# Kernel tuning notes

Measured on AMD Instinct MI355X. Metric: run time of the kernel, lower is better.

The kernel has to match this reference:

```python
import jax, jax.numpy as jnp
import numpy as np

B, N, M, K = 1, 200000, 100000, 16
C_IN, C_OUT, GFL, HEADS = 64, 128, 32, 8
C4 = C_OUT // 4          # 32, unary1 bottleneck width
C_MID = 16               # weightnet output channels


def _lin(key, fan_in, fan_out):
    return jax.random.normal(key, (fan_in, fan_out), jnp.float32) / np.sqrt(fan_in)


def setup_inputs() -> dict:
    key = jax.random.key(0)
    ks = jax.random.split(key, 20)
    return {
        'dense_xyz': jax.random.normal(ks[0], (B, N, 3), jnp.float32),
        'dense_feats': jax.random.normal(ks[1], (B, N, C_IN), jnp.float32),
        'dense_xyz_norm': jax.random.normal(ks[2], (B, N, 3), jnp.float32),
        'sparse_xyz': jax.random.normal(ks[3], (B, M, 3), jnp.float32),
        'sparse_xyz_norm': jax.random.normal(ks[4], (B, M, 3), jnp.float32),
        'vi_features': jax.random.normal(ks[5], (B, M, K, 12), jnp.float32),
        'nei_inds': jax.random.randint(ks[6], (B, M, K), 0, N),
        # unary1: in -> out/4 (Linear + BN(eval,init) + LeakyReLU(0.1))
        'w_unary1': _lin(ks[7], C_IN, C4), 'b_unary1': jnp.zeros((C4,), jnp.float32),
        # guidance_unary: out/4 -> GFL, no relu
        'w_gu': _lin(ks[8], C4, GFL), 'b_gu': jnp.zeros((GFL,), jnp.float32),
        # mlp_conv: 12 -> GFL (positional encoding on VI features)
        'w_pe': _lin(ks[9], 12, GFL), 'b_pe': jnp.zeros((GFL,), jnp.float32),
        # MultiHeadGuidance (subtraction): 2*GFL -> 8 -> HEADS
        'w_g1': _lin(ks[10], 2 * GFL, 8), 'b_g1': jnp.zeros((8,), jnp.float32),
        'w_g2': _lin(ks[11], 8, HEADS), 'b_g2': jnp.zeros((HEADS,), jnp.float32),
        # WeightNet: 12 -> 8 -> 8 -> 16, relu after each
        'w_wn1': _lin(ks[12], 12, 8), 'b_wn1': jnp.zeros((8,), jnp.float32),
        'w_wn2': _lin(ks[13], 8, 8), 'b_wn2': jnp.zeros((8,), jnp.float32),
        'w_wn3': _lin(ks[14], 8, C_MID), 'b_wn3': jnp.zeros((C_MID,), jnp.float32),
        # linear: out/4 * C_MID -> out/2
        'w_lin': _lin(ks[15], C4 * C_MID, C_OUT // 2), 'b_lin': jnp.zeros((C_OUT // 2,), jnp.float32),
        # unary2: out/2 -> out, no relu
        'w_u2': _lin(ks[16], C_OUT // 2, C_OUT), 'b_u2': jnp.zeros((C_OUT,), jnp.float32),
        # unary_shortcut: in -> out, no relu
        'w_sc': _lin(ks[17], C_IN, C_OUT), 'b_sc': jnp.zeros((C_OUT,), jnp.float32),
    }


def _gather(points, idx):
    # points: [B, N, C], idx: [B, M, K] int -> [B, M, K, C]
    return jax.vmap(lambda p, i: p[i])(points, idx)


def reference(dense_xyz, dense_feats, dense_xyz_norm, sparse_xyz, sparse_xyz_norm,
              vi_features, nei_inds,
              w_unary1, b_unary1, w_gu, b_gu, w_pe, b_pe,
              w_g1, b_g1, w_g2, b_g2,
              w_wn1, b_wn1, w_wn2, b_wn2, w_wn3, b_wn3,
              w_lin, b_lin, w_u2, b_u2, w_sc, b_sc):
    b, m, k = nei_inds.shape
    # unary1 (Linear+BN@init folds to Linear, LeakyReLU 0.1)
    feats_x = jax.nn.leaky_relu(dense_feats @ w_unary1 + b_unary1, 0.1)  # [B,N,C4]
    # USE_VI=True with precomputed vi_features -> weightNetInput = vi_features
    weightnet_input = vi_features                                        # [B,M,K,12]
    feat_pe = jax.nn.relu(weightnet_input @ w_pe + b_pe)                 # [B,M,K,GFL]
    guidance_x = feats_x @ w_gu + b_gu                                   # [B,N,GFL] (no_relu)
    gathered_g = _gather(guidance_x, nei_inds)                           # [B,M,K,GFL]
    g_feat = jnp.concatenate([gathered_g, feat_pe], axis=-1)             # [B,M,K,2*GFL]
    # subtraction guidance: query - max-pooled key over neighborhood
    scores = g_feat - jnp.max(g_feat, axis=2, keepdims=True)
    scores = jax.nn.relu(scores @ w_g1 + b_g1)
    scores = jax.nn.sigmoid(scores @ w_g2 + b_g2)                        # [B,M,K,H]
    gathered_feat = _gather(feats_x, nei_inds)                           # [B,M,K,C4]
    nf = gathered_feat.reshape(b, m, k, HEADS, C4 // HEADS) * scores[..., None]
    nf = nf.reshape(b, m, k, C4)
    # WeightNet on VI features
    w = jax.nn.relu(weightnet_input @ w_wn1 + b_wn1)
    w = jax.nn.relu(w @ w_wn2 + b_wn2)
    w = jax.nn.relu(w @ w_wn3 + b_wn3)                                   # [B,M,K,C_MID]
    # weighted neighbor aggregation: feat^T @ weights per point
    agg = jnp.einsum('bmkc,bmkw->bmcw', nf, w).reshape(b, m, C4 * C_MID)
    out = jax.nn.relu(agg @ w_lin + b_lin)                               # [B,M,out/2]
    out = out @ w_u2 + b_u2                                              # unary2, no relu
    # strided shortcut: max-pool dense feats over neighborhood, then unary
    sparse_feats = jnp.max(_gather(dense_feats, nei_inds), axis=2)       # [B,M,C_IN]
    shortcut = sparse_feats @ w_sc + b_sc
    return jax.nn.leaky_relu(out + shortcut, 0.1)                        # [B,M,C_OUT]
```

## Files before the change

### kernel.cpp

```cpp
#include <hip/hip_runtime.h>
#include <math.h>

typedef __attribute__((ext_vector_type(8))) __bf16 bf16x8;
typedef __attribute__((ext_vector_type(4))) __bf16 bf16x4;
typedef __attribute__((ext_vector_type(4))) float f32x4;
typedef __attribute__((ext_vector_type(8))) unsigned short ushort8;
typedef __attribute__((ext_vector_type(2))) _Float16 h2;

__device__ __forceinline__ float fdot2(h2 a, h2 b, float c) {
#if __has_builtin(__builtin_amdgcn_fdot2)
    return __builtin_amdgcn_fdot2(a, b, c, false);
#else
    return c + (float)a[0] * (float)b[0] + (float)a[1] * (float)b[1];
#endif
}

__device__ __forceinline__ h2 h2max(h2 a, h2 b) {
#if __has_builtin(__builtin_elementwise_max)
    return __builtin_elementwise_max(a, b);
#else
    h2 r; r[0] = a[0] > b[0] ? a[0] : b[0]; r[1] = a[1] > b[1] ? a[1] : b[1]; return r;
#endif
}

__device__ __forceinline__ h2 rowmax16h(h2 x) {
    int xi = __builtin_bit_cast(int, x);
    int y;
    y = __builtin_amdgcn_update_dpp(0, xi, 0x128, 0xf, 0xf, true);
    x = h2max(x, __builtin_bit_cast(h2, y)); xi = __builtin_bit_cast(int, x);
    y = __builtin_amdgcn_update_dpp(0, xi, 0x124, 0xf, 0xf, true);
    x = h2max(x, __builtin_bit_cast(h2, y)); xi = __builtin_bit_cast(int, x);
    y = __builtin_amdgcn_update_dpp(0, xi, 0x122, 0xf, 0xf, true);
    x = h2max(x, __builtin_bit_cast(h2, y)); xi = __builtin_bit_cast(int, x);
    y = __builtin_amdgcn_update_dpp(0, xi, 0x121, 0xf, 0xf, true);
    x = h2max(x, __builtin_bit_cast(h2, y));
    return x;
}

__device__ __forceinline__ unsigned int packh2(float a, float b) {
    h2 v = { (_Float16)a, (_Float16)b };
    return __builtin_bit_cast(unsigned int, v);
}

__global__ void prep_kernel(const float* __restrict__ wlin,
                            const float* __restrict__ wu2,
                            const float* __restrict__ wsc,
                            const float* __restrict__ w1,
                            const float* __restrict__ wg,
                            const float* __restrict__ wg1,
                            const float* __restrict__ wpe,
                            const float* __restrict__ wn1,
                            const float* __restrict__ wn2,
                            const float* __restrict__ wn3,
                            const float* __restrict__ wg2,
                            __bf16* __restrict__ wlinT,
                            __bf16* __restrict__ wu2T,
                            __bf16* __restrict__ wscT,
                            __bf16* __restrict__ w1Th,
                            __bf16* __restrict__ w1Tl,
                            __bf16* __restrict__ wgT,
                            unsigned int* __restrict__ pk)
{
    const int B0 = 64 * 512;
    const int B1 = B0 + 128 * 64;
    const int B2 = B1 + 128 * 64;
    const int B3 = B2 + 32 * 64;
    const int B4 = B3 + 32 * 32;
    const int B5 = B4 + 256;
    const int B6 = B5 + 192;
    const int B7 = B6 + 48;
    const int B8 = B7 + 32;
    const int B9 = B8 + 64;
    const int B10 = B9 + 32;
    int i = blockIdx.x * 256 + threadIdx.x;
    if (i < B0) {
        int l = i >> 9, k = i & 511;
        wlinT[i] = (__bf16)wlin[k * 64 + l];
    } else if (i < B1) {
        int j = i - B0; int co = j >> 6, kk = j & 63;
        wu2T[j] = (__bf16)wu2[kk * 128 + co];
    } else if (i < B2) {
        int j = i - B1; int co = j >> 6, kk = j & 63;
        wscT[j] = (__bf16)wsc[kk * 128 + co];
    } else if (i < B3) {
        int j = i - B2; int c = j >> 6, k = j & 63;
        float v = w1[k * 32 + c];
        __bf16 h = (__bf16)v;
        w1Th[j] = h;
        w1Tl[j] = (__bf16)(v - (float)h);
    } else if (i < B4) {
        int j = i - B3; int c = j >> 5, k = j & 31;
        wgT[j] = (__bf16)wg[k * 32 + c];
    } else if (i < B5) {
        int j2 = i - B4; int t = j2 >> 3, j = j2 & 7;
        pk[j2] = packh2(wg1[(2 * t) * 8 + j], wg1[(2 * t + 1) * 8 + j]);
    } else if (i < B6) {
        int j2 = i - B5; int t = j2 >> 5, c = j2 & 31;
        pk[256 + j2] = packh2(wpe[(2 * t) * 32 + c], wpe[(2 * t + 1) * 32 + c]);
    } else if (i < B7) {
        int j2 = i - B6; int t = j2 >> 3, j = j2 & 7;
        pk[448 + j2] = packh2(wn1[(2 * t) * 8 + j], wn1[(2 * t + 1) * 8 + j]);
    } else if (i < B8) {
        int j2 = i - B7; int t = j2 >> 3, j = j2 & 7;
        pk[496 + j2] = packh2(wn2[(2 * t) * 8 + j], wn2[(2 * t + 1) * 8 + j]);
    } else if (i < B9) {
        int j2 = i - B8; int t = j2 >> 4, j = j2 & 15;
        pk[528 + j2] = packh2(wn3[(2 * t) * 16 + j], wn3[(2 * t + 1) * 16 + j]);
    } else if (i < B10) {
        int j2 = i - B9; int t = j2 >> 3, j = j2 & 7;
        pk[592 + j2] = packh2(wg2[(2 * t) * 8 + j], wg2[(2 * t + 1) * 8 + j]);
    }
}

__global__ __launch_bounds__(256) void feats_kernel(
    const float* __restrict__ df,
    const __bf16* __restrict__ w1Th, const __bf16* __restrict__ w1Tl,
    const float* __restrict__ b1,
    const __bf16* __restrict__ wgT, const float* __restrict__ bg,
    __bf16* __restrict__ fxb, unsigned short* __restrict__ gxh,
    __bf16* __restrict__ dfb, int N)
{
    __shared__ unsigned short sFx[4][16][40];
    int t = threadIdx.x;
    int wv = t >> 6, ln = t & 63;
    int row = ln & 15, quad = ln >> 4;
    long n0 = (long)blockIdx.x * 64 + wv * 16;
    long n = n0 + row;
    bool ok = n < (long)N;

    const float4* dp = (const float4*)(df + (ok ? n * 64 : 0));
    float4 f00 = dp[quad * 2 + 0], f01 = dp[quad * 2 + 1];
    float4 f10 = dp[8 + quad * 2 + 0], f11 = dp[8 + quad * 2 + 1];
    float s0[8] = {f00.x, f00.y, f00.z, f00.w, f01.x, f01.y, f01.z, f01.w};
    float s1[8] = {f10.x, f10.y, f10.z, f10.w, f11.x, f11.y, f11.z, f11.w};
    bf16x8 aH0, aL0, aH1, aL1;
#pragma unroll
    for (int e = 0; e < 8; e++) {
        __bf16 h = (__bf16)s0[e]; aH0[e] = h; aL0[e] = (__bf16)(s0[e] - (float)h);
        __bf16 g = (__bf16)s1[e]; aH1[e] = g; aL1[e] = (__bf16)(s1[e] - (float)g);
    }
    if (ok) {
        *(bf16x8*)(dfb + n * 64 + quad * 8) = aH0;
        *(bf16x8*)(dfb + n * 64 + 32 + quad * 8) = aH1;
    }

    const __bf16* bh = w1Th + (row * 64 + quad * 8);
    const __bf16* bl = w1Tl + (row * 64 + quad * 8);
    f32x4 acc0 = {0.f, 0.f, 0.f, 0.f}, acc1 = {0.f, 0.f, 0.f, 0.f};
    {
        bf16x8 bH00 = *(const bf16x8*)(bh);
        bf16x8 bH01 = *(const bf16x8*)(bh + 32);
        bf16x8 bH10 = *(const bf16x8*)(bh + 16 * 64);
        bf16x8 bH11 = *(const bf16x8*)(bh + 16 * 64 + 32);
        bf16x8 bL00 = *(const bf16x8*)(bl);
        bf16x8 bL01 = *(const bf16x8*)(bl + 32);
        bf16x8 bL10 = *(const bf16x8*)(bl + 16 * 64);
        bf16x8 bL11 = *(const bf16x8*)(bl + 16 * 64 + 32);
        acc0 = __builtin_amdgcn_mfma_f32_16x16x32_bf16(aH0, bH00, acc0, 0, 0, 0);
        acc0 = __builtin_amdgcn_mfma_f32_16x16x32_bf16(aH1, bH01, acc0, 0, 0, 0);
        acc0 = __builtin_amdgcn_mfma_f32_16x16x32_bf16(aL0, bH00, acc0, 0, 0, 0);
        acc0 = __builtin_amdgcn_mfma_f32_16x16x32_bf16(aL1, bH01, acc0, 0, 0, 0);
        acc0 = __builtin_amdgcn_mfma_f32_16x16x32_bf16(aH0, bL00, acc0, 0, 0, 0);
        acc0 = __builtin_amdgcn_mfma_f32_16x16x32_bf16(aH1, bL01, acc0, 0, 0, 0);
        acc1 = __builtin_amdgcn_mfma_f32_16x16x32_bf16(aH0, bH10, acc1, 0, 0, 0);
        acc1 = __builtin_amdgcn_mfma_f32_16x16x32_bf16(aH1, bH11, acc1, 0, 0, 0);
        acc1 = __builtin_amdgcn_mfma_f32_16x16x32_bf16(aL0, bH10, acc1, 0, 0, 0);
        acc1 = __builtin_amdgcn_mfma_f32_16x16x32_bf16(aL1, bH11, acc1, 0, 0, 0);
        acc1 = __builtin_amdgcn_mfma_f32_16x16x32_bf16(aH0, bL10, acc1, 0, 0, 0);
        acc1 = __builtin_amdgcn_mfma_f32_16x16x32_bf16(aH1, bL11, acc1, 0, 0, 0);
    }
    {
        float bb0 = b1[row], bb1 = b1[16 + row];
#pragma unroll
        for (int r = 0; r < 4; r++) {
            float x0 = acc0[r] + bb0; x0 = x0 > 0.f ? x0 : 0.1f * x0;
            float x1 = acc1[r] + bb1; x1 = x1 > 0.f ? x1 : 0.1f * x1;
            sFx[wv][quad * 4 + r][row] = __builtin_bit_cast(unsigned short, (__bf16)x0);
            sFx[wv][quad * 4 + r][16 + row] = __builtin_bit_cast(unsigned short, (__bf16)x1);
        }
    }
    __builtin_amdgcn_s_waitcnt(0);

    f32x4 g0 = {0.f, 0.f, 0.f, 0.f}, g1 = {0.f, 0.f, 0.f, 0.f};
    {
        bf16x8 a2 = __builtin_bit_cast(bf16x8, *(const ushort8*)(&sFx[wv][row][quad * 8]));
        bf16x8 b20 = *(const bf16x8*)(wgT + row * 32 + quad * 8);
        bf16x8 b21 = *(const bf16x8*)(wgT + (16 + row) * 32 + quad * 8);
        g0 = __builtin_amdgcn_mfma_f32_16x16x32_bf16(a2, b20, g0, 0, 0, 0);
        g1 = __builtin_amdgcn_mfma_f32_16x16x32_bf16(a2, b21, g1, 0, 0, 0);
    }
    {
        int r16 = ln >> 2, seg = ln & 3;
        ushort8 vfx = *(const ushort8*)(&sFx[wv][r16][seg * 8]);
        long nn = n0 + r16;
        if (nn < (long)N) *(ushort8*)((unsigned short*)fxb + nn * 32 + seg * 8) = vfx;
    }
    {
        float bb0 = bg[row], bb1 = bg[16 + row];
#pragma unroll
        for (int r = 0; r < 4; r++) {
            sFx[wv][quad * 4 + r][row] = __builtin_bit_cast(unsigned short, (_Float16)(g0[r] + bb0));
            sFx[wv][quad * 4 + r][16 + row] = __builtin_bit_cast(unsigned short, (_Float16)(g1[r] + bb1));
        }
    }
    __builtin_amdgcn_s_waitcnt(0);
    {
        int r16 = ln >> 2, seg = ln & 3;
        ushort8 vg = *(const ushort8*)(&sFx[wv][r16][seg * 8]);
        long nn = n0 + r16;
        if (nn < (long)N) *(ushort8*)(gxh + nn * 32 + seg * 8) = vg;
    }
}

struct SmemU {
    union {
        struct { __bf16 nfF[16 * 512]; __bf16 w3A[16 * 256]; } a;
        __bf16 aggB[16][520];
    };
};

__global__ __launch_bounds__(256, 5) void pcf_kernel(
    const float* __restrict__ vi, const int* __restrict__ nei,
    const __bf16* __restrict__ fxb, const unsigned short* __restrict__ gxh,
    const __bf16* __restrict__ dfb,
    const unsigned int* __restrict__ pk,
    const float* __restrict__ bpe,
    const float* __restrict__ bg1, const float* __restrict__ bg2,
    const float* __restrict__ bn1, const float* __restrict__ bn2,
    const float* __restrict__ bn3,
    const __bf16* __restrict__ wlinT, const float* __restrict__ blin,
    const __bf16* __restrict__ wu2T, const float* __restrict__ bu2,
    const __bf16* __restrict__ wscT, const float* __restrict__ bsc,
    float* __restrict__ out, int M)
{
    __shared__ SmemU U;
    __shared__ __bf16 sO[16][72];
    __shared__ __bf16 sS[16][72];
    __shared__ int sInd[16][16];

    const unsigned int* wg1P = pk;
    const unsigned int* wpeP = pk + 256;
    const unsigned int* wn1P = pk + 448;
    const unsigned int* wn2P = pk + 496;
    const unsigned int* wn3P = pk + 528;
    const unsigned int* wg2P = pk + 592;

    int t = threadIdx.x;
    int p = t >> 4, q = t & 15;
    long mbase = (long)blockIdx.x * 16;
    long m = mbase + p;
    bool okm = m < (long)M;
    int ind = okm ? nei[m * 16 + q] : 0;
    sInd[p][q] = ind;

    h2 vh[6];
    {
        const float4* v4 = (const float4*)(vi + (okm ? (m * 16 + q) * 12 : 0));
        float4 a = v4[0], b = v4[1], cc = v4[2];
        vh[0] = (h2){(_Float16)a.x, (_Float16)a.y};
        vh[1] = (h2){(_Float16)a.z, (_Float16)a.w};
        vh[2] = (h2){(_Float16)b.x, (_Float16)b.y};
        vh[3] = (h2){(_Float16)b.z, (_Float16)b.w};
        vh[4] = (h2){(_Float16)cc.x, (_Float16)cc.y};
        vh[5] = (h2){(_Float16)cc.z, (_Float16)cc.w};
    }
    {
        float wa[8];
#pragma unroll
        for (int j = 0; j < 8; j++) {
            float a = bn1[j];
#pragma unroll
            for (int tt2 = 0; tt2 < 6; tt2++)
                a = fdot2(vh[tt2], __builtin_bit_cast(h2, wn1P[tt2 * 8 + j]), a);
            wa[j] = fmaxf(a, 0.f);
        }
        h2 wah[4];
#pragma unroll
        for (int tt2 = 0; tt2 < 4; tt2++)
            wah[tt2] = (h2){(_Float16)wa[2 * tt2], (_Float16)wa[2 * tt2 + 1]};
        float wb[8];
#pragma unroll
        for (int j = 0; j < 8; j++) {
            float a = bn2[j];
#pragma unroll
            for (int tt2 = 0; tt2 < 4; tt2++)
                a = fdot2(wah[tt2], __builtin_bit_cast(h2, wn2P[tt2 * 8 + j]), a);
            wb[j] = fmaxf(a, 0.f);
        }
        h2 wbh[4];
#pragma unroll
        for (int tt2 = 0; tt2 < 4; tt2++)
            wbh[tt2] = (h2){(_Float16)wb[2 * tt2], (_Float16)wb[2 * tt2 + 1]};
        int swz = (p & 3) << 4;
        int kb = (q >> 3) * 128 + (q & 7);
#pragma unroll
        for (int j = 0; j < 16; j++) {
            float a = bn3[j];
#pragma unroll
            for (int tt2 = 0; tt2 < 4; tt2++)
                a = fdot2(wbh[tt2], __builtin_bit_cast(h2, wn3P[tt2 * 16 + j]), a);
            U.a.w3A[p * 256 + ((kb + j * 8) ^ swz)] = (__bf16)fmaxf(a, 0.f);
        }
    }
    h2 peh[16];
#pragma unroll
    for (int c2 = 0; c2 < 16; c2++) {
        float a0 = bpe[2 * c2], a1 = bpe[2 * c2 + 1];
#pragma unroll
        for (int tt2 = 0; tt2 < 6; tt2++) {
            a0 = fdot2(vh[tt2], __builtin_bit_cast(h2, wpeP[tt2 * 32 + 2 * c2]), a0);
            a1 = fdot2(vh[tt2], __builtin_bit_cast(h2, wpeP[tt2 * 32 + 2 * c2 + 1]), a1);
        }
        peh[c2] = (h2){(_Float16)fmaxf(a0, 0.f), (_Float16)fmaxf(a1, 0.f)};
    }
    h2 gdh[16];
    {
        const unsigned int* gu = (const unsigned int*)(gxh + (long)ind * 32);
#pragma unroll
        for (int tt2 = 0; tt2 < 16; tt2++)
            gdh[tt2] = __builtin_bit_cast(h2, gu[tt2]);
    }
    float s1[8];
#pragma unroll
    for (int j = 0; j < 8; j++) s1[j] = bg1[j];
#pragma unroll
    for (int tt2 = 0; tt2 < 32; tt2++) {
        h2 g2 = (tt2 < 16) ? gdh[tt2] : peh[tt2 - 16];
        h2 m2 = rowmax16h(g2);
        h2 sub = g2 - m2;
#pragma unroll
        for (int j = 0; j < 8; j++)
            s1[j] = fdot2(sub, __builtin_bit_cast(h2, wg1P[tt2 * 8 + j]), s1[j]);
    }
    h2 s1h[4];
#pragma unroll
    for (int tt2 = 0; tt2 < 4; tt2++)
        s1h[tt2] = (h2){(_Float16)fmaxf(s1[2 * tt2], 0.f), (_Float16)fmaxf(s1[2 * tt2 + 1], 0.f)};
    float s2[8];
#pragma unroll
    for (int j = 0; j < 8; j++) {
        float a = bg2[j];
#pragma unroll
        for (int tt2 = 0; tt2 < 4; tt2++)
            a = fdot2(s1h[tt2], __builtin_bit_cast(h2, wg2P[tt2 * 8 + j]), a);
        s2[j] = 1.f / (1.f + __expf(-a));
    }
    {
        const bf16x8* f8 = (const bf16x8*)(fxb + (long)ind * 32);
        int swz = (p & 3) << 4;
#pragma unroll
        for (int g = 0; g < 4; g++) {
            bf16x8 f = f8[g];
            float sA = s2[2 * g], sB = s2[2 * g + 1];
#pragma unroll
            for (int e = 0; e < 8; e++) {
                int c = g * 8 + e;
                float val = (float)f[e] * (e < 4 ? sA : sB);
                U.a.nfF[p * 512 + ((((c >> 4) * 256) + (c & 15) * 16 + q) ^ swz)] = (__bf16)val;
            }
        }
    }
    {
        float4 mx = make_float4(-1e30f, -1e30f, -1e30f, -1e30f);
#pragma unroll
        for (int kk = 0; kk < 16; kk++) {
            int ik = sInd[p][kk];
            bf16x4 d = *(const bf16x4*)(dfb + (long)ik * 64 + q * 4);
            mx.x = fmaxf(mx.x, (float)d[0]); mx.y = fmaxf(mx.y, (float)d[1]);
            mx.z = fmaxf(mx.z, (float)d[2]); mx.w = fmaxf(mx.w, (float)d[3]);
        }
        bf16x4 pkk;
        pkk[0] = (__bf16)mx.x; pkk[1] = (__bf16)mx.y; pkk[2] = (__bf16)mx.z; pkk[3] = (__bf16)mx.w;
        *(bf16x4*)(&sS[p][q * 4]) = pkk;
    }

    {
        int wv2 = t >> 6, ln2 = t & 63;
        int col = ln2 & 15, quad = ln2 >> 4;
        bf16x8 z8 = {};
        bf16x4 dpk[4][2];
#pragma unroll
        for (int pp = 0; pp < 4; pp++) {
            int p2 = wv2 * 4 + pp;
            int swz = (p2 & 3) << 4;
            bf16x8 afr = z8, bf0 = z8, bf1 = z8;
            if (quad < 2) {
                afr = *(const bf16x8*)(&U.a.w3A[p2 * 256 + ((quad * 128 + col * 8) ^ swz)]);
                bf0 = *(const bf16x8*)(&U.a.nfF[p2 * 512 + ((col * 16 + quad * 8) ^ swz)]);
                bf1 = *(const bf16x8*)(&U.a.nfF[p2 * 512 + ((256 + col * 16 + quad * 8) ^ swz)]);
            }
            f32x4 ac0 = {0.f, 0.f, 0.f, 0.f}, ac1 = {0.f, 0.f, 0.f, 0.f};
            ac0 = __builtin_amdgcn_mfma_f32_16x16x32_bf16(afr, bf0, ac0, 0, 0, 0);
            ac1 = __builtin_amdgcn_mfma_f32_16x16x32_bf16(afr, bf1, ac1, 0, 0, 0);
#pragma unroll
            for (int r = 0; r < 4; r++) {
                dpk[pp][0][r] = (__bf16)ac0[r];
                dpk[pp][1][r] = (__bf16)ac1[r];
            }
        }
        __syncthreads();
#pragma unroll
        for (int pp = 0; pp < 4; pp++) {
            int p2 = wv2 * 4 + pp;
            *(bf16x4*)(&U.aggB[p2][col * 16 + quad * 4]) = dpk[pp][0];
            *(bf16x4*)(&U.aggB[p2][(16 + col) * 16 + quad * 4]) = dpk[pp][1];
        }
    }
    __syncthreads();

    {
        int wv = t >> 6, ln = t & 63;
        int n = ln & 15, quad = ln >> 4;
        const __bf16* Bp = wlinT + ((wv * 16 + n) * 512 + quad * 8);
        f32x4 acc = {0.f, 0.f, 0.f, 0.f};
#pragma unroll
        for (int kk = 0; kk < 16; kk++) {
            bf16x8 a = *(const bf16x8*)(&U.aggB[n][kk * 32 + quad * 8]);
            bf16x8 b = *(const bf16x8*)(Bp + kk * 32);
            acc = __builtin_amdgcn_mfma_f32_16x16x32_bf16(a, b, acc, 0, 0, 0);
        }
        int col = wv * 16 + n;
        float bl = blin[col];
#pragma unroll
        for (int r = 0; r < 4; r++) {
            int row = quad * 4 + r;
            sO[row][col] = (__bf16)fmaxf(acc[r] + bl, 0.f);
        }
    }
    __syncthreads();

    {
        int wv = t >> 6, ln = t & 63;
        int n = ln & 15, quad = ln >> 4;
        bf16x8 aO0 = *(const bf16x8*)(&sO[n][quad * 8]);
        bf16x8 aO1 = *(const bf16x8*)(&sO[n][32 + quad * 8]);
        bf16x8 aS0 = *(const bf16x8*)(&sS[n][quad * 8]);
        bf16x8 aS1 = *(const bf16x8*)(&sS[n][32 + quad * 8]);
#pragma unroll
        for (int tt = 0; tt < 2; tt++) {
            int T = wv * 2 + tt;
            int col = T * 16 + n;
            const __bf16* B1 = wu2T + (col * 64 + quad * 8);
            const __bf16* B2 = wscT + (col * 64 + quad * 8);
            f32x4 acc = {0.f, 0.f, 0.f, 0.f};
            acc = __builtin_amdgcn_mfma_f32_16x16x32_bf16(aO0, *(const bf16x8*)(B1), acc, 0, 0, 0);
            acc = __builtin_amdgcn_mfma_f32_16x16x32_bf16(aO1, *(const bf16x8*)(B1 + 32), acc, 0, 0, 0);
            acc = __builtin_amdgcn_mfma_f32_16x16x32_bf16(aS0, *(const bf16x8*)(B2), acc, 0, 0, 0);
            acc = __builtin_amdgcn_mfma_f32_16x16x32_bf16(aS1, *(const bf16x8*)(B2 + 32), acc, 0, 0, 0);
            float bb = bu2[col] + bsc[col];
#pragma unroll
            for (int r = 0; r < 4; r++) {
                long mm = mbase + quad * 4 + r;
                if (mm < (long)M) {
                    float x = acc[r] + bb;
                    out[mm * 128 + col] = x > 0.f ? x : 0.1f * x;
                }
            }
        }
    }
}

extern "C" void kernel_launch(void* const* d_in, const int* in_sizes, int n_in,
                              void* d_out, int out_size, void* d_ws, size_t ws_size,
                              hipStream_t stream)
{
    const float* dense_feats = (const float*)d_in[1];
    const float* vi    = (const float*)d_in[5];
    const int*   nei   = (const int*)d_in[6];
    const float* w_u1  = (const float*)d_in[7];
    const float* b_u1  = (const float*)d_in[8];
    const float* w_gu  = (const float*)d_in[9];
    const float* b_gu  = (const float*)d_in[10];
    const float* w_pe  = (const float*)d_in[11];
    const float* b_pe  = (const float*)d_in[12];
    const float* w_g1  = (const float*)d_in[13];
    const float* b_g1  = (const float*)d_in[14];
    const float* w_g2  = (const float*)d_in[15];
    const float* b_g2  = (const float*)d_in[16];
    const float* w_wn1 = (const float*)d_in[17];
    const float* b_wn1 = (const float*)d_in[18];
    const float* w_wn2 = (const float*)d_in[19];
    const float* b_wn2 = (const float*)d_in[20];
    const float* w_wn3 = (const float*)d_in[21];
    const float* b_wn3 = (const float*)d_in[22];
    const float* w_lin = (const float*)d_in[23];
    const float* b_lin = (const float*)d_in[24];
    const float* w_u2  = (const float*)d_in[25];
    const float* b_u2  = (const float*)d_in[26];
    const float* w_sc  = (const float*)d_in[27];
    const float* b_sc  = (const float*)d_in[28];

    int N = in_sizes[1] / 64;
    int M = in_sizes[6] / 16;

    __bf16* fxb  = (__bf16*)d_ws;
    unsigned short* gxh = (unsigned short*)(fxb + (size_t)N * 32);
    __bf16* dfb  = (__bf16*)(gxh + (size_t)N * 32);
    __bf16* wlinT = dfb + (size_t)N * 64;
    __bf16* wu2T  = wlinT + 64 * 512;
    __bf16* wscT  = wu2T + 128 * 64;
    __bf16* w1Th  = wscT + 128 * 64;
    __bf16* w1Tl  = w1Th + 32 * 64;
    __bf16* wgT   = w1Tl + 32 * 64;
    unsigned int* pk = (unsigned int*)(wgT + 32 * 32);

    const int prep_items = 64 * 512 + 2 * 128 * 64 + 2 * 32 * 64 + 32 * 32 + 624;
    prep_kernel<<<(prep_items + 255) / 256, 256, 0, stream>>>(
        w_lin, w_u2, w_sc, w_u1, w_gu, w_g1, w_pe, w_wn1, w_wn2, w_wn3, w_g2,
        wlinT, wu2T, wscT, w1Th, w1Tl, wgT, pk);

    feats_kernel<<<(N + 63) / 64, 256, 0, stream>>>(
        dense_feats, w1Th, w1Tl, b_u1, wgT, b_gu, fxb, gxh, dfb, N);

    pcf_kernel<<<(M + 15) / 16, 256, 0, stream>>>(
        vi, nei, fxb, gxh, dfb, pk,
        b_pe, b_g1, b_g2, b_wn1, b_wn2, b_wn3,
        wlinT, b_lin, wu2T, b_u2, wscT, b_sc,
        (float*)d_out, M);
}
```

Baseline: 369.7 us.

## Raise pcf occupancy, hoist neighbor gathers, and process two tiles per feats block

The feats kernel now handles 128 rows per block in two passes and loads the weight fragments and biases once per block instead of once per 64 rows. In the pcf kernel the neighbor gathers of guidance and features are issued at kernel start so their latency overlaps the positional-encoding math. The shared index table is replaced with a 16-lane shuffle, and sO is folded into the shared-memory union, cutting LDS per block so launch bounds can rise from 5 to 6 blocks per CU. Holding the hoisted gathers in registers raises register pressure, which may cause spills under the tighter launch bound.

```diff
diff --git a/kernel.cpp b/kernel.cpp
--- a/kernel.cpp
+++ b/kernel.cpp
@@ -124,38 +124,46 @@
     int t = threadIdx.x;
     int wv = t >> 6, ln = t & 63;
     int row = ln & 15, quad = ln >> 4;
-    long n0 = (long)blockIdx.x * 64 + wv * 16;
-    long n = n0 + row;
-    bool ok = n < (long)N;
-
-    const float4* dp = (const float4*)(df + (ok ? n * 64 : 0));
-    float4 f00 = dp[quad * 2 + 0], f01 = dp[quad * 2 + 1];
-    float4 f10 = dp[8 + quad * 2 + 0], f11 = dp[8 + quad * 2 + 1];
-    float s0[8] = {f00.x, f00.y, f00.z, f00.w, f01.x, f01.y, f01.z, f01.w};
-    float s1[8] = {f10.x, f10.y, f10.z, f10.w, f11.x, f11.y, f11.z, f11.w};
-    bf16x8 aH0, aL0, aH1, aL1;
-#pragma unroll
-    for (int e = 0; e < 8; e++) {
-        __bf16 h = (__bf16)s0[e]; aH0[e] = h; aL0[e] = (__bf16)(s0[e] - (float)h);
-        __bf16 g = (__bf16)s1[e]; aH1[e] = g; aL1[e] = (__bf16)(s1[e] - (float)g);
-    }
-    if (ok) {
-        *(bf16x8*)(dfb + n * 64 + quad * 8) = aH0;
-        *(bf16x8*)(dfb + n * 64 + 32 + quad * 8) = aH1;
-    }
+    long B0 = (long)blockIdx.x * 128;
 
     const __bf16* bh = w1Th + (row * 64 + quad * 8);
     const __bf16* bl = w1Tl + (row * 64 + quad * 8);
-    f32x4 acc0 = {0.f, 0.f, 0.f, 0.f}, acc1 = {0.f, 0.f, 0.f, 0.f};
-    {
-        bf16x8 bH00 = *(const bf16x8*)(bh);
-        bf16x8 bH01 = *(const bf16x8*)(bh + 32);
-        bf16x8 bH10 = *(const bf16x8*)(bh + 16 * 64);
-        bf16x8 bH11 = *(const bf16x8*)(bh + 16 * 64 + 32);
-        bf16x8 bL00 = *(const bf16x8*)(bl);
-        bf16x8 bL01 = *(const bf16x8*)(bl + 32);
-        bf16x8 bL10 = *(const bf16x8*)(bl + 16 * 64);
-        bf16x8 bL11 = *(const bf16x8*)(bl + 16 * 64 + 32);
+    bf16x8 bH00 = *(const bf16x8*)(bh);
+    bf16x8 bH01 = *(const bf16x8*)(bh + 32);
+    bf16x8 bH10 = *(const bf16x8*)(bh + 16 * 64);
+    bf16x8 bH11 = *(const bf16x8*)(bh + 16 * 64 + 32);
+    bf16x8 bL00 = *(const bf16x8*)(bl);
+    bf16x8 bL01 = *(const bf16x8*)(bl + 32);
+    bf16x8 bL10 = *(const bf16x8*)(bl + 16 * 64);
+    bf16x8 bL11 = *(const bf16x8*)(bl + 16 * 64 + 32);
+    bf16x8 b20 = *(const bf16x8*)(wgT + row * 32 + quad * 8);
+    bf16x8 b21 = *(const bf16x8*)(wgT + (16 + row) * 32 + quad * 8);
+    float bb0 = b1[row], bb1 = b1[16 + row];
+    float bgg0 = bg[row], bgg1 = bg[16 + row];
+
+#pragma unroll
+    for (int half = 0; half < 2; ++half) {
+        long n0 = B0 + half * 64 + wv * 16;
+        long n = n0 + row;
+        bool ok = n < (long)N;
+
+        const float4* dp = (const float4*)(df + (ok ? n * 64 : 0));
+        float4 f00 = dp[quad * 2 + 0], f01 = dp[quad * 2 + 1];
+        float4 f10 = dp[8 + quad * 2 + 0], f11 = dp[8 + quad * 2 + 1];
+        float s0[8] = {f00.x, f00.y, f00.z, f00.w, f01.x, f01.y, f01.z, f01.w};
+        float s1[8] = {f10.x, f10.y, f10.z, f10.w, f11.x, f11.y, f11.z, f11.w};
+        bf16x8 aH0, aL0, aH1, aL1;
+#pragma unroll
+        for (int e = 0; e < 8; e++) {
+            __bf16 h = (__bf16)s0[e]; aH0[e] = h; aL0[e] = (__bf16)(s0[e] - (float)h);
+            __bf16 g = (__bf16)s1[e]; aH1[e] = g; aL1[e] = (__bf16)(s1[e] - (float)g);
+        }
+        if (ok) {
+            *(bf16x8*)(dfb + n * 64 + quad * 8) = aH0;
+            *(bf16x8*)(dfb + n * 64 + 32 + quad * 8) = aH1;
+        }
+
+        f32x4 acc0 = {0.f, 0.f, 0.f, 0.f}, acc1 = {0.f, 0.f, 0.f, 0.f};
         acc0 = __builtin_amdgcn_mfma_f32_16x16x32_bf16(aH0, bH00, acc0, 0, 0, 0);
         acc0 = __builtin_amdgcn_mfma_f32_16x16x32_bf16(aH1, bH01, acc0, 0, 0, 0);
         acc0 = __builtin_amdgcn_mfma_f32_16x16x32_bf16(aL0, bH00, acc0, 0, 0, 0);
@@ -168,9 +176,7 @@
         acc1 = __builtin_amdgcn_mfma_f32_16x16x32_bf16(aL1, bH11, acc1, 0, 0, 0);
         acc1 = __builtin_amdgcn_mfma_f32_16x16x32_bf16(aH0, bL10, acc1, 0, 0, 0);
         acc1 = __builtin_amdgcn_mfma_f32_16x16x32_bf16(aH1, bL11, acc1, 0, 0, 0);
-    }
-    {
-        float bb0 = b1[row], bb1 = b1[16 + row];
+
 #pragma unroll
         for (int r = 0; r < 4; r++) {
             float x0 = acc0[r] + bb0; x0 = x0 > 0.f ? x0 : 0.1f * x0;
@@ -178,48 +184,41 @@
             sFx[wv][quad * 4 + r][row] = __builtin_bit_cast(unsigned short, (__bf16)x0);
             sFx[wv][quad * 4 + r][16 + row] = __builtin_bit_cast(unsigned short, (__bf16)x1);
         }
-    }
-    __builtin_amdgcn_s_waitcnt(0);
-
-    f32x4 g0 = {0.f, 0.f, 0.f, 0.f}, g1 = {0.f, 0.f, 0.f, 0.f};
-    {
-        bf16x8 a2 = __builtin_bit_cast(bf16x8, *(const ushort8*)(&sFx[wv][row][quad * 8]));
-        bf16x8 b20 = *(const bf16x8*)(wgT + row * 32 + quad * 8);
-        bf16x8 b21 = *(const bf16x8*)(wgT + (16 + row) * 32 + quad * 8);
-        g0 = __builtin_amdgcn_mfma_f32_16x16x32_bf16(a2, b20, g0, 0, 0, 0);
-        g1 = __builtin_amdgcn_mfma_f32_16x16x32_bf16(a2, b21, g1, 0, 0, 0);
-    }
-    {
-        int r16 = ln >> 2, seg = ln & 3;
-        ushort8 vfx = *(const ushort8*)(&sFx[wv][r16][seg * 8]);
-        long nn = n0 + r16;
-        if (nn < (long)N) *(ushort8*)((unsigned short*)fxb + nn * 32 + seg * 8) = vfx;
-    }
-    {
-        float bb0 = bg[row], bb1 = bg[16 + row];
+
+        f32x4 g0 = {0.f, 0.f, 0.f, 0.f}, g1 = {0.f, 0.f, 0.f, 0.f};
+        {
+            bf16x8 a2 = __builtin_bit_cast(bf16x8, *(const ushort8*)(&sFx[wv][row][quad * 8]));
+            g0 = __builtin_amdgcn_mfma_f32_16x16x32_bf16(a2, b20, g0, 0, 0, 0);
+            g1 = __builtin_amdgcn_mfma_f32_16x16x32_bf16(a2, b21, g1, 0, 0, 0);
+        }
+        {
+            int r16 = ln >> 2, seg = ln & 3;
+            ushort8 vfx = *(const ushort8*)(&sFx[wv][r16][seg * 8]);
+            long nn = n0 + r16;
+            if (nn < (long)N) *(ushort8*)((unsigned short*)fxb + nn * 32 + seg * 8) = vfx;
+        }
 #pragma unroll
         for (int r = 0; r < 4; r++) {
-            sFx[wv][quad * 4 + r][row] = __builtin_bit_cast(unsigned short, (_Float16)(g0[r] + bb0));
-            sFx[wv][quad * 4 + r][16 + row] = __builtin_bit_cast(unsigned short, (_Float16)(g1[r] + bb1));
-        }
-    }
-    __builtin_amdgcn_s_waitcnt(0);
-    {
-        int r16 = ln >> 2, seg = ln & 3;
-        ushort8 vg = *(const ushort8*)(&sFx[wv][r16][seg * 8]);
-        long nn = n0 + r16;
-        if (nn < (long)N) *(ushort8*)(gxh + nn * 32 + seg * 8) = vg;
+            sFx[wv][quad * 4 + r][row] = __builtin_bit_cast(unsigned short, (_Float16)(g0[r] + bgg0));
+            sFx[wv][quad * 4 + r][16 + row] = __builtin_bit_cast(unsigned short, (_Float16)(g1[r] + bgg1));
+        }
+        {
+            int r16 = ln >> 2, seg = ln & 3;
+            ushort8 vg = *(const ushort8*)(&sFx[wv][r16][seg * 8]);
+            long nn = n0 + r16;
+            if (nn < (long)N) *(ushort8*)(gxh + nn * 32 + seg * 8) = vg;
+        }
     }
 }
 
 struct SmemU {
     union {
         struct { __bf16 nfF[16 * 512]; __bf16 w3A[16 * 256]; } a;
-        __bf16 aggB[16][520];
+        struct { __bf16 aggB[16][520]; __bf16 sO[16][72]; } b;
     };
 };
 
-__global__ __launch_bounds__(256, 5) void pcf_kernel(
+__global__ __launch_bounds__(256, 6) void pcf_kernel(
     const float* __restrict__ vi, const int* __restrict__ nei,
     const __bf16* __restrict__ fxb, const unsigned short* __restrict__ gxh,
     const __bf16* __restrict__ dfb,
@@ -234,9 +233,7 @@
     float* __restrict__ out, int M)
 {
     __shared__ SmemU U;
-    __shared__ __bf16 sO[16][72];
     __shared__ __bf16 sS[16][72];
-    __shared__ int sInd[16][16];
 
     const unsigned int* wg1P = pk;
     const unsigned int* wpeP = pk + 256;
@@ -251,8 +248,19 @@
     long m = mbase + p;
     bool okm = m < (long)M;
     int ind = okm ? nei[m * 16 + q] : 0;
-    sInd[p][q] = ind;
-
+
+    h2 gdh[16];
+    {
+        const unsigned int* gu = (const unsigned int*)(gxh + (long)ind * 32);
+#pragma unroll
+        for (int i = 0; i < 16; i++) gdh[i] = __builtin_bit_cast(h2, gu[i]);
+    }
+    bf16x8 fxr[4];
+    {
+        const bf16x8* f8 = (const bf16x8*)(fxb + (long)ind * 32);
+#pragma unroll
+        for (int g = 0; g < 4; g++) fxr[g] = f8[g];
+    }
     h2 vh[6];
     {
         const float4* v4 = (const float4*)(vi + (okm ? (m * 16 + q) * 12 : 0));
@@ -313,13 +321,6 @@
         }
         peh[c2] = (h2){(_Float16)fmaxf(a0, 0.f), (_Float16)fmaxf(a1, 0.f)};
     }
-    h2 gdh[16];
-    {
-        const unsigned int* gu = (const unsigned int*)(gxh + (long)ind * 32);
-#pragma unroll
-        for (int tt2 = 0; tt2 < 16; tt2++)
-            gdh[tt2] = __builtin_bit_cast(h2, gu[tt2]);
-    }
     float s1[8];
 #pragma unroll
     for (int j = 0; j < 8; j++) s1[j] = bg1[j];
@@ -346,11 +347,10 @@
         s2[j] = 1.f / (1.f + __expf(-a));
     }
     {
-        const bf16x8* f8 = (const bf16x8*)(fxb + (long)ind * 32);
         int swz = (p & 3) << 4;
 #pragma unroll
         for (int g = 0; g < 4; g++) {
-            bf16x8 f = f8[g];
+            bf16x8 f = fxr[g];
             float sA = s2[2 * g], sB = s2[2 * g + 1];
 #pragma unroll
             for (int e = 0; e < 8; e++) {
@@ -364,7 +364,7 @@
         float4 mx = make_float4(-1e30f, -1e30f, -1e30f, -1e30f);
 #pragma unroll
         for (int kk = 0; kk < 16; kk++) {
-            int ik = sInd[p][kk];
+            int ik = __shfl(ind, kk, 16);
             bf16x4 d = *(const bf16x4*)(dfb + (long)ik * 64 + q * 4);
             mx.x = fmaxf(mx.x, (float)d[0]); mx.y = fmaxf(mx.y, (float)d[1]);
             mx.z = fmaxf(mx.z, (float)d[2]); mx.w = fmaxf(mx.w, (float)d[3]);
@@ -402,8 +402,8 @@
 #pragma unroll
         for (int pp = 0; pp < 4; pp++) {
             int p2 = wv2 * 4 + pp;
-            *(bf16x4*)(&U.aggB[p2][col * 16 + quad * 4]) = dpk[pp][0];
-            *(bf16x4*)(&U.aggB[p2][(16 + col) * 16 + quad * 4]) = dpk[pp][1];
+            *(bf16x4*)(&U.b.aggB[p2][col * 16 + quad * 4]) = dpk[pp][0];
+            *(bf16x4*)(&U.b.aggB[p2][(16 + col) * 16 + quad * 4]) = dpk[pp][1];
         }
     }
     __syncthreads();
@@ -415,7 +415,7 @@
         f32x4 acc = {0.f, 0.f, 0.f, 0.f};
 #pragma unroll
         for (int kk = 0; kk < 16; kk++) {
-            bf16x8 a = *(const bf16x8*)(&U.aggB[n][kk * 32 + quad * 8]);
+            bf16x8 a = *(const bf16x8*)(&U.b.aggB[n][kk * 32 + quad * 8]);
             bf16x8 b = *(const bf16x8*)(Bp + kk * 32);
             acc = __builtin_amdgcn_mfma_f32_16x16x32_bf16(a, b, acc, 0, 0, 0);
         }
@@ -424,7 +424,7 @@
 #pragma unroll
         for (int r = 0; r < 4; r++) {
             int row = quad * 4 + r;
-            sO[row][col] = (__bf16)fmaxf(acc[r] + bl, 0.f);
+            U.b.sO[row][col] = (__bf16)fmaxf(acc[r] + bl, 0.f);
         }
     }
     __syncthreads();
@@ -432,8 +432,8 @@
     {
         int wv = t >> 6, ln = t & 63;
         int n = ln & 15, quad = ln >> 4;
-        bf16x8 aO0 = *(const bf16x8*)(&sO[n][quad * 8]);
-        bf16x8 aO1 = *(const bf16x8*)(&sO[n][32 + quad * 8]);
+        bf16x8 aO0 = *(const bf16x8*)(&U.b.sO[n][quad * 8]);
+        bf16x8 aO1 = *(const bf16x8*)(&U.b.sO[n][32 + quad * 8]);
         bf16x8 aS0 = *(const bf16x8*)(&sS[n][quad * 8]);
         bf16x8 aS1 = *(const bf16x8*)(&sS[n][32 + quad * 8]);
 #pragma unroll
@@ -509,7 +509,7 @@
         w_lin, w_u2, w_sc, w_u1, w_gu, w_g1, w_pe, w_wn1, w_wn2, w_wn3, w_g2,
         wlinT, wu2T, wscT, w1Th, w1Tl, wgT, pk);
 
-    feats_kernel<<<(N + 63) / 64, 256, 0, stream>>>(
+    feats_kernel<<<(N + 127) / 128, 256, 0, stream>>>(
         dense_feats, w1Th, w1Tl, b_u1, wgT, b_gu, fxb, gxh, dfb, N);
 
     pcf_kernel<<<(M + 15) / 16, 256, 0, stream>>>(
```

Result: faster. 350.5 us (-5.2%).
